# Performance work log

Hardware: AMD Instinct MI355X
Metric: run time of the kernel (lower is better)

## Reference

```python
import jax, jax.numpy as jnp
import numpy as np

CAPACITY = 0.7
TEMP = 0.5          # initial_temp, never annealed (global_step=None path)
LB_WEIGHT = 0.005
Z_WEIGHT = 5e-06
EPS = 1e-10


def setup_inputs() -> dict:
    key = jax.random.key(0)
    k1, k2, k3 = jax.random.split(key, 3)
    B, S, H = 4, 8192, 2048
    return {
        "hidden_states": jax.random.normal(k1, (B, S, H), dtype=jnp.float32),
        "active_mask": jnp.ones((B, S), dtype=bool),
        "u": jax.random.uniform(k2, (B, S), dtype=jnp.float32),
        # router: nn.Linear(H, 1), weight ~ N(0, 0.02), bias = 0
        "w": jax.random.normal(k3, (H,), dtype=jnp.float32) * 0.02,
        "b": jnp.zeros((), dtype=jnp.float32),
    }


def reference(hidden_states, active_mask, u, w, b):
    B, S = active_mask.shape
    N = B * S
    # mask is all-True by construction -> num_active = N, k static
    num_active = N
    k = max(1, min(int(CAPACITY * num_active), num_active))

    # scores = router(hidden).squeeze(-1)  -> [B,S]
    scores = jnp.einsum("bsh,h->bs", hidden_states, w) + b
    scores = jnp.where(active_mask, scores, -jnp.inf)

    # gumbel noise from uniform u (matches torch.rand_like path)
    gumbel = -jnp.log(-jnp.log(u + EPS) + EPS)
    noisy = ((scores + gumbel) / TEMP).reshape(-1)  # [N]

    _, idx = jax.lax.top_k(noisy, k)
    ffn_mask = jnp.zeros((N,), dtype=bool).at[idx].set(True)
    ffn_mask = ffn_mask.reshape(B, S) & active_mask

    # aux losses (masked reductions over active tokens)
    maskf = active_mask.astype(jnp.float32)
    na = maskf.sum()
    safe_scores = jnp.where(active_mask, scores, 0.0)
    f = ffn_mask.astype(jnp.float32).sum() / na
    p = (jax.nn.sigmoid(safe_scores) * maskf).sum() / na
    lb_loss = (f - CAPACITY) ** 2 + (p - CAPACITY) ** 2
    z_loss = (safe_scores ** 2 * maskf).sum() / na
    aux_loss = LB_WEIGHT * lb_loss + Z_WEIGHT * z_loss

    return ffn_mask, aux_loss
```

## Files before the change

### kernel.cpp

```cpp
#include <hip/hip_runtime.h>
#include <math.h>

#define NTOK 32768
#define HDIM 2048
#define K_SEL 22937
#define EPS_F 1e-10f
#define NBLK 2048

__global__ __launch_bounds__(256) void score_kernel(
    const float* __restrict__ hidden,
    const float* __restrict__ u,
    const float* __restrict__ w,
    const float* __restrict__ b,
    unsigned int* __restrict__ keys,
    float* __restrict__ pp,
    float* __restrict__ zz)
{
    const int wave = threadIdx.x >> 6;
    const int lane = threadIdx.x & 63;
    const int tok0 = blockIdx.x * 16 + wave * 4;

    const float4* __restrict__ w4 = (const float4*)w;
    float4 wr[8];
    #pragma unroll
    for (int j = 0; j < 8; ++j) wr[j] = w4[j * 64 + lane];

    float p_acc = 0.0f, z_acc = 0.0f;
    #pragma unroll
    for (int t = 0; t < 4; ++t) {
        const int token = tok0 + t;
        const float4* __restrict__ hrow = (const float4*)(hidden + (size_t)token * HDIM);
        float sum = 0.0f;
        #pragma unroll
        for (int j = 0; j < 8; ++j) {
            const float4 hv = hrow[j * 64 + lane];
            sum += hv.x * wr[j].x + hv.y * wr[j].y + hv.z * wr[j].z + hv.w * wr[j].w;
        }
        #pragma unroll
        for (int off = 32; off > 0; off >>= 1)
            sum += __shfl_down(sum, off, 64);
        if (lane == 0) {
            const float score = sum + b[0];
            const float uu = u[token];
            const float g = -logf(-logf(uu + EPS_F) + EPS_F);
            const float noisy = (score + g) * 2.0f;
            const unsigned int bits = __float_as_uint(noisy);
            keys[token] = (bits & 0x80000000u) ? ~bits : (bits | 0x80000000u);
            p_acc += 1.0f / (1.0f + expf(-score));
            z_acc += score * score;
        }
    }

    __shared__ float red_p[4], red_z[4];
    if (lane == 0) { red_p[wave] = p_acc; red_z[wave] = z_acc; }
    __syncthreads();
    if (threadIdx.x == 0) {
        pp[blockIdx.x] = red_p[0] + red_p[1] + red_p[2] + red_p[3];
        zz[blockIdx.x] = red_z[0] + red_z[1] + red_z[2] + red_z[3];
    }
}

__global__ __launch_bounds__(1024) void select_kernel(
    const unsigned int* __restrict__ keys,
    const float* __restrict__ pp,
    const float* __restrict__ zz,
    float* __restrict__ out)
{
    __shared__ unsigned int wcnt[16];
    __shared__ float wredp[16], wredz[16];
    __shared__ unsigned int wtot[16], woff[16];

    const int t = threadIdx.x;
    const int lane = t & 63;
    const int wid = t >> 6;
    const int base = t * 32;

    unsigned int myk[32];
    #pragma unroll
    for (int j = 0; j < 32; ++j) myk[j] = keys[base + j];

    unsigned int tau = 0u;
    for (int bit = 31; bit >= 0; --bit) {
        const unsigned int cand = tau | (1u << bit);
        unsigned int c = 0u;
        #pragma unroll
        for (int j = 0; j < 32; ++j) c += (myk[j] >= cand) ? 1u : 0u;
        #pragma unroll
        for (int off = 32; off > 0; off >>= 1) c += __shfl_down(c, off, 64);
        if (lane == 0) wcnt[wid] = c;
        __syncthreads();
        unsigned int tot = 0u;
        #pragma unroll
        for (int i = 0; i < 16; ++i) tot += wcnt[i];
        if (tot >= (unsigned int)K_SEL) tau = cand;
        __syncthreads();
    }

    unsigned int cgt = 0u;
    #pragma unroll
    for (int j = 0; j < 32; ++j) cgt += (myk[j] > tau) ? 1u : 0u;
    unsigned int cg = cgt;
    #pragma unroll
    for (int off = 32; off > 0; off >>= 1) cg += __shfl_down(cg, off, 64);
    if (lane == 0) wcnt[wid] = cg;
    __syncthreads();
    unsigned int tot_gt = 0u;
    #pragma unroll
    for (int i = 0; i < 16; ++i) tot_gt += wcnt[i];
    const unsigned int needed = (unsigned int)K_SEL - tot_gt;

    unsigned int ceq = 0u;
    #pragma unroll
    for (int j = 0; j < 32; ++j) ceq += (myk[j] == tau) ? 1u : 0u;
    unsigned int v = ceq;
    #pragma unroll
    for (int off = 1; off < 64; off <<= 1) {
        const unsigned int n = __shfl_up(v, off, 64);
        if (lane >= off) v += n;
    }
    __syncthreads();
    if (lane == 63) wtot[wid] = v;
    __syncthreads();
    if (t == 0) {
        unsigned int run = 0u;
        for (int i = 0; i < 16; ++i) { woff[i] = run; run += wtot[i]; }
    }
    __syncthreads();
    unsigned int rank = woff[wid] + (v - ceq);

    #pragma unroll
    for (int j = 0; j < 32; ++j) {
        const unsigned int kk = myk[j];
        float val;
        if (kk > tau) {
            val = 1.0f;
        } else if (kk == tau) {
            val = (rank < needed) ? 1.0f : 0.0f;
            rank++;
        } else {
            val = 0.0f;
        }
        out[base + j] = val;
    }

    float lp = 0.0f, lz = 0.0f;
    if (t < 1024) {
        lp = pp[t] + pp[t + 1024];
        lz = zz[t] + zz[t + 1024];
    }
    #pragma unroll
    for (int off = 32; off > 0; off >>= 1) {
        lp += __shfl_down(lp, off, 64);
        lz += __shfl_down(lz, off, 64);
    }
    if (lane == 0) { wredp[wid] = lp; wredz[wid] = lz; }
    __syncthreads();
    if (t == 0) {
        float sp = 0.0f, sz = 0.0f;
        for (int i = 0; i < 16; ++i) { sp += wredp[i]; sz += wredz[i]; }
        const float na = (float)NTOK;
        const float f = (float)K_SEL / na;
        const float p = sp / na;
        const float z = sz / na;
        const float d1 = f - 0.7f;
        const float d2 = p - 0.7f;
        out[NTOK] = 0.005f * (d1 * d1 + d2 * d2) + 5e-6f * z;
    }
}

extern "C" void kernel_launch(void* const* d_in, const int* in_sizes, int n_in,
                              void* d_out, int out_size, void* d_ws, size_t ws_size,
                              hipStream_t stream) {
    const float* hidden = (const float*)d_in[0];
    const float* u = (const float*)d_in[2];
    const float* w = (const float*)d_in[3];
    const float* b = (const float*)d_in[4];
    float* out = (float*)d_out;

    const size_t KEYS_BYTES = (size_t)NTOK * sizeof(unsigned int);
    const size_t PART_BYTES = (size_t)NBLK * sizeof(float);

    unsigned int* keys;
    float *pp, *zz;
    if (ws_size >= KEYS_BYTES + 2 * PART_BYTES) {
        keys = (unsigned int*)d_ws;
        pp = (float*)((char*)d_ws + KEYS_BYTES);
        zz = pp + NBLK;
    } else {
        keys = (unsigned int*)d_out;
        pp = (float*)d_ws;
        zz = pp + NBLK;
    }

    score_kernel<<<NBLK, 256, 0, stream>>>(hidden, u, w, b, keys, pp, zz);
    select_kernel<<<1, 1024, 0, stream>>>(keys, pp, zz, out);
}
```

Measured before the change: 409.2 us.

## Double-buffer row loads in scorer and stage select I/O through shared memory

The score kernel now handles 8 rows per wave with double-buffered float4 loads and batched shuffle reductions, and launches half as many blocks. The select kernel loads keys and stores the mask through a padded LDS buffer, so global accesses become coalesced uint4/float4 instead of strided 32-element-per-thread runs. Both changes target memory inefficiency. In exchange they raise register pressure in the scorer and add several block-wide barriers in the single-block select kernel.

```diff
diff --git a/kernel.cpp b/kernel.cpp
--- a/kernel.cpp
+++ b/kernel.cpp
@@ -5,7 +5,7 @@
 #define HDIM 2048
 #define K_SEL 22937
 #define EPS_F 1e-10f
-#define NBLK 2048
+#define SBLK 1024
 
 __global__ __launch_bounds__(256) void score_kernel(
     const float* __restrict__ hidden,
@@ -18,41 +18,62 @@
 {
     const int wave = threadIdx.x >> 6;
     const int lane = threadIdx.x & 63;
-    const int tok0 = blockIdx.x * 16 + wave * 4;
+    const int row0 = blockIdx.x * 32 + wave * 8;
 
     const float4* __restrict__ w4 = (const float4*)w;
     float4 wr[8];
     #pragma unroll
     for (int j = 0; j < 8; ++j) wr[j] = w4[j * 64 + lane];
 
-    float p_acc = 0.0f, z_acc = 0.0f;
-    #pragma unroll
-    for (int t = 0; t < 4; ++t) {
-        const int token = tok0 + t;
-        const float4* __restrict__ hrow = (const float4*)(hidden + (size_t)token * HDIM);
-        float sum = 0.0f;
+    const float4* __restrict__ rowp = (const float4*)(hidden + (size_t)row0 * HDIM);
+
+    float sums[8];
+    float4 buf[2][8];
+    #pragma unroll
+    for (int j = 0; j < 8; ++j) buf[0][j] = rowp[j * 64 + lane];
+
+    #pragma unroll
+    for (int r = 0; r < 8; ++r) {
+        const int cur = r & 1, nxt = cur ^ 1;
+        if (r < 7) {
+            #pragma unroll
+            for (int j = 0; j < 8; ++j)
+                buf[nxt][j] = rowp[(r + 1) * 512 + j * 64 + lane];
+        }
+        float s = 0.0f;
         #pragma unroll
         for (int j = 0; j < 8; ++j) {
-            const float4 hv = hrow[j * 64 + lane];
-            sum += hv.x * wr[j].x + hv.y * wr[j].y + hv.z * wr[j].z + hv.w * wr[j].w;
-        }
-        #pragma unroll
-        for (int off = 32; off > 0; off >>= 1)
-            sum += __shfl_down(sum, off, 64);
-        if (lane == 0) {
-            const float score = sum + b[0];
-            const float uu = u[token];
+            const float4 hv = buf[cur][j];
+            s += hv.x * wr[j].x + hv.y * wr[j].y + hv.z * wr[j].z + hv.w * wr[j].w;
+        }
+        sums[r] = s;
+    }
+
+    #pragma unroll
+    for (int off = 32; off > 0; off >>= 1) {
+        #pragma unroll
+        for (int r = 0; r < 8; ++r)
+            sums[r] += __shfl_down(sums[r], off, 64);
+    }
+
+    __shared__ float red_p[4], red_z[4];
+    if (lane == 0) {
+        const float bias = b[0];
+        float p_acc = 0.0f, z_acc = 0.0f;
+        #pragma unroll
+        for (int r = 0; r < 8; ++r) {
+            const float score = sums[r] + bias;
+            const float uu = u[row0 + r];
             const float g = -logf(-logf(uu + EPS_F) + EPS_F);
             const float noisy = (score + g) * 2.0f;
             const unsigned int bits = __float_as_uint(noisy);
-            keys[token] = (bits & 0x80000000u) ? ~bits : (bits | 0x80000000u);
+            keys[row0 + r] = (bits & 0x80000000u) ? ~bits : (bits | 0x80000000u);
             p_acc += 1.0f / (1.0f + expf(-score));
             z_acc += score * score;
         }
-    }
-
-    __shared__ float red_p[4], red_z[4];
-    if (lane == 0) { red_p[wave] = p_acc; red_z[wave] = z_acc; }
+        red_p[wave] = p_acc;
+        red_z[wave] = z_acc;
+    }
     __syncthreads();
     if (threadIdx.x == 0) {
         pp[blockIdx.x] = red_p[0] + red_p[1] + red_p[2] + red_p[3];
@@ -66,6 +87,7 @@
     const float* __restrict__ zz,
     float* __restrict__ out)
 {
+    __shared__ unsigned int sbuf[8448];
     __shared__ unsigned int wcnt[16];
     __shared__ float wredp[16], wredz[16];
     __shared__ unsigned int wtot[16], woff[16];
@@ -73,11 +95,30 @@
     const int t = threadIdx.x;
     const int lane = t & 63;
     const int wid = t >> 6;
-    const int base = t * 32;
 
     unsigned int myk[32];
-    #pragma unroll
-    for (int j = 0; j < 32; ++j) myk[j] = keys[base + j];
+    for (int p = 0; p < 4; ++p) {
+        #pragma unroll
+        for (int q = 0; q < 2; ++q) {
+            const int v4idx = t + 1024 * q;
+            const int e = 4 * v4idx;
+            const uint4 kv = ((const uint4*)(keys + 8192 * p))[v4idx];
+            *((uint4*)&sbuf[e + (e >> 5)]) = kv;
+        }
+        __syncthreads();
+        const int c = t - 256 * p;
+        if (c >= 0 && c < 256) {
+            #pragma unroll
+            for (int j = 0; j < 8; ++j) {
+                const uint4 kv = *((const uint4*)&sbuf[33 * c + 4 * j]);
+                myk[4 * j + 0] = kv.x;
+                myk[4 * j + 1] = kv.y;
+                myk[4 * j + 2] = kv.z;
+                myk[4 * j + 3] = kv.w;
+            }
+        }
+        __syncthreads();
+    }
 
     unsigned int tau = 0u;
     for (int bit = 31; bit >= 0; --bit) {
@@ -128,26 +169,37 @@
     __syncthreads();
     unsigned int rank = woff[wid] + (v - ceq);
 
-    #pragma unroll
-    for (int j = 0; j < 32; ++j) {
-        const unsigned int kk = myk[j];
-        float val;
-        if (kk > tau) {
-            val = 1.0f;
-        } else if (kk == tau) {
-            val = (rank < needed) ? 1.0f : 0.0f;
-            rank++;
-        } else {
-            val = 0.0f;
-        }
-        out[base + j] = val;
-    }
-
-    float lp = 0.0f, lz = 0.0f;
-    if (t < 1024) {
-        lp = pp[t] + pp[t + 1024];
-        lz = zz[t] + zz[t + 1024];
-    }
+    for (int p = 0; p < 4; ++p) {
+        const int c = t - 256 * p;
+        if (c >= 0 && c < 256) {
+            #pragma unroll
+            for (int j = 0; j < 32; ++j) {
+                const unsigned int kk = myk[j];
+                float val;
+                if (kk > tau) {
+                    val = 1.0f;
+                } else if (kk == tau) {
+                    val = (rank < needed) ? 1.0f : 0.0f;
+                    rank++;
+                } else {
+                    val = 0.0f;
+                }
+                const int e = 32 * c + j;
+                ((float*)sbuf)[e + (e >> 5)] = val;
+            }
+        }
+        __syncthreads();
+        #pragma unroll
+        for (int q = 0; q < 2; ++q) {
+            const int v4idx = t + 1024 * q;
+            const int e = 4 * v4idx;
+            const float4 fv = *((const float4*)&((float*)sbuf)[e + (e >> 5)]);
+            ((float4*)(out + 8192 * p))[v4idx] = fv;
+        }
+        __syncthreads();
+    }
+
+    float lp = pp[t], lz = zz[t];
     #pragma unroll
     for (int off = 32; off > 0; off >>= 1) {
         lp += __shfl_down(lp, off, 64);
@@ -178,20 +230,20 @@
     float* out = (float*)d_out;
 
     const size_t KEYS_BYTES = (size_t)NTOK * sizeof(unsigned int);
-    const size_t PART_BYTES = (size_t)NBLK * sizeof(float);
+    const size_t PART_BYTES = (size_t)SBLK * sizeof(float);
 
     unsigned int* keys;
     float *pp, *zz;
     if (ws_size >= KEYS_BYTES + 2 * PART_BYTES) {
         keys = (unsigned int*)d_ws;
         pp = (float*)((char*)d_ws + KEYS_BYTES);
-        zz = pp + NBLK;
+        zz = pp + SBLK;
     } else {
         keys = (unsigned int*)d_out;
         pp = (float*)d_ws;
-        zz = pp + NBLK;
-    }
-
-    score_kernel<<<NBLK, 256, 0, stream>>>(hidden, u, w, b, keys, pp, zz);
+        zz = pp + SBLK;
+    }
+
+    score_kernel<<<SBLK, 256, 0, stream>>>(hidden, u, w, b, keys, pp, zz);
     select_kernel<<<1, 1024, 0, stream>>>(keys, pp, zz, out);
 }
```

Result: no change. 404.9 us (-1.1%).
